# Optimization experiments

Hardware: AMD Instinct MI355X
Metric: run time of the kernel (lower is better)

Reference implementation:

```python
import jax, jax.numpy as jnp
import numpy as np

B, T, D, H = 32, 2048, 256, 256


def setup_inputs() -> dict:
    key = jax.random.key(0)
    ks = jax.random.split(key, 7)
    s = 1.0 / np.sqrt(H)  # PyTorch GRUCell default init scale
    x = jax.random.normal(ks[0], (B, T, D), jnp.float32)
    seg = jax.random.randint(ks[1], (B, T), 0, 2, jnp.int32)  # 1 = continue segment, 0 = boundary (write+reset)
    lengths = jax.random.randint(ks[2], (B,), T // 2, T, jnp.int32)
    W_ih = jax.random.uniform(ks[3], (3 * H, D), jnp.float32, -s, s)
    W_hh = jax.random.uniform(ks[4], (3 * H, H), jnp.float32, -s, s)
    b_ih = jax.random.uniform(ks[5], (3 * H,), jnp.float32, -s, s)
    b_hh = jax.random.uniform(ks[6], (3 * H,), jnp.float32, -s, s)
    return {"x": x, "seg": seg, "lengths": lengths,
            "W_ih": W_ih, "W_hh": W_hh, "b_ih": b_ih, "b_hh": b_hh}


def gru_cell(xt, h, W_ih, W_hh, b_ih, b_hh):
    # PyTorch GRUCell math
    gi = xt @ W_ih.T + b_ih          # [B, 3H]
    gh = h @ W_hh.T + b_hh           # [B, 3H]
    i_r, i_z, i_n = jnp.split(gi, 3, axis=-1)
    h_r, h_z, h_n = jnp.split(gh, 3, axis=-1)
    r = jax.nn.sigmoid(i_r + h_r)
    z = jax.nn.sigmoid(i_z + h_z)
    n = jnp.tanh(i_n + r * h_n)
    return (1.0 - z) * n + z * h


def reference(x, seg, lengths, W_ih, W_hh, b_ih, b_hh):
    Bn, Tn, _ = x.shape
    Hn = W_hh.shape[1]
    barange = jnp.arange(Bn)

    def step(carry, inp):
        h, idx, out = carry
        xt, seg_t, t = inp
        h_new = gru_cell(xt, h, W_ih, W_hh, b_ih, b_hh)
        # write h at per-example position idx where segment boundary and t < length
        write = (seg_t == 0) & (t < lengths)                     # [B] bool
        cur = out[barange, idx]                                  # [B, H]
        out = out.at[barange, idx].set(jnp.where(write[:, None], h_new, cur))
        idx = idx + write.astype(idx.dtype)
        # reset hidden to zero at segment boundaries (seg==0)
        h = seg_t.astype(h_new.dtype)[:, None] * h_new
        return (h, idx, out), None

    h0 = jnp.zeros((Bn, Hn), x.dtype)
    idx0 = jnp.zeros((Bn,), jnp.int32)
    # static max output length = Tn (original uses data-dependent max; we pad to T)
    out0 = jnp.zeros((Bn, Tn, Hn), x.dtype)
    (h, idx, out), _ = jax.lax.scan(
        step, (h0, idx0, out0),
        (jnp.transpose(x, (1, 0, 2)), seg.T, jnp.arange(Tn)))
    return out, idx
```

## Files before the change

### kernel.cpp

```cpp
#include <hip/hip_runtime.h>
#include <cstdint>
#include <cstddef>

#define TT 2048
#define BB 32
#define DD 256
#define HH 256
#define G3 768

using bf16x8 = __attribute__((ext_vector_type(8))) short;
using f32x4  = __attribute__((ext_vector_type(4))) float;

static const size_t REC_OFF = 64;
static const size_t BIH_OFF = 64 + (size_t)65536 * 16;
static const size_t BHH_OFF = BIH_OFF + (size_t)G3 * DD * 2;

__device__ __forceinline__ uint16_t f2bf(float v) {
    unsigned int u = __float_as_uint(v);
    u += 0x7FFF + ((u >> 16) & 1);
    return (uint16_t)(u >> 16);
}
__device__ __forceinline__ float bf2f(uint16_t h) {
    return __uint_as_float(((unsigned int)h) << 16);
}
__device__ __forceinline__ float sigmoidf_(float v) {
    return 1.f / (1.f + __expf(-v));
}
__device__ __forceinline__ float tanhf_(float v) {
    v = fminf(fmaxf(v, -30.f), 30.f);
    float e = __expf(-2.f * v);
    return (1.f - e) / (1.f + e);
}

__global__ void k_prep(const float* __restrict__ Wih, const float* __restrict__ Whh,
                       uint16_t* __restrict__ Bih, uint16_t* __restrict__ Bhh) {
    int i = blockIdx.x * 256 + threadIdx.x;
    if (i < G3 * DD) { Bih[i] = f2bf(Wih[i]); Bhh[i] = f2bf(Whh[i]); }
}

__global__ void k_meta(const int* __restrict__ seg, const int* __restrict__ lengths,
                       int4* __restrict__ recs, int* __restrict__ counters,
                       float* __restrict__ outIdx) {
    int b = blockIdx.x;
    int tid = threadIdx.x;
    int len = lengths[b];
    const int* s = seg + (size_t)b * TT;
    const int CH = TT / 256;
    int t0 = tid * CH;

    int cnt = 0;
    for (int t = t0; t < t0 + CH; ++t)
        cnt += (s[t] == 0 && t < len) ? 1 : 0;

    __shared__ int part[256];
    __shared__ int base;
    part[tid] = cnt;
    __syncthreads();
    if (tid == 0) {
        int run = 0;
        for (int i = 0; i < 256; ++i) { int v = part[i]; part[i] = run; run += v; }
        base = atomicAdd(&counters[0], run);
        outIdx[b] = (float)run;
    }
    __syncthreads();

    int run = part[tid];
    for (int t = t0; t < t0 + CH; ++t) {
        if (s[t] == 0 && t < len) {
            int ss = t - 1;
            while (ss >= 0 && s[ss] != 0) --ss;
            recs[base + run] = make_int4(b, ss + 1, t, run);
            ++run;
        }
    }
}

__global__ __launch_bounds__(512) void k_main(
    const float* __restrict__ x,
    const uint16_t* __restrict__ Bih, const uint16_t* __restrict__ Bhh,
    const float* __restrict__ b_ih, const float* __restrict__ b_hh,
    const int4* __restrict__ recs, int* __restrict__ counters,
    float* __restrict__ out)
{
    __shared__ __attribute__((aligned(16))) uint16_t xAhi[16 * 256];
    __shared__ __attribute__((aligned(16))) uint16_t xAlo[16 * 256];
    __shared__ __attribute__((aligned(16))) uint16_t hAhi[16 * 256];
    __shared__ __attribute__((aligned(16))) uint16_t hAlo[16 * 256];
    __shared__ int rb[16], rt[16], re[16], rp[16], alive[16];
    __shared__ int anyAliveS, nsegS;

    const int tid  = threadIdx.x;
    const int lane = tid & 63;
    const int w    = tid >> 6;
    const int lcol = lane & 15;
    const int lk8  = (lane >> 4) << 3;
    const int lrow4 = (lane >> 4) << 2;

    for (int i = tid; i < 16 * 256; i += 512) { hAhi[i] = 0; hAlo[i] = 0; }
    if (tid < 16) { alive[tid] = 0; rb[tid] = 0; rt[tid] = 0; re[tid] = -1; rp[tid] = 0; }
    if (tid == 0) nsegS = counters[0];
    __syncthreads();
    const int nseg = nsegS;

    float bR[2], bZ[2], bIN[2], bHN[2];
    #pragma unroll
    for (int ct = 0; ct < 2; ++ct) {
        int c = w * 32 + ct * 16 + lcol;
        bR[ct]  = b_ih[c]       + b_hh[c];
        bZ[ct]  = b_ih[256 + c] + b_hh[256 + c];
        bIN[ct] = b_ih[512 + c];
        bHN[ct] = b_hh[512 + c];
    }
    float hm[2][4] = {{0.f,0.f,0.f,0.f},{0.f,0.f,0.f,0.f}};

    const int srow = tid >> 5;
    const int scs  = tid & 31;

    for (;;) {
        if (tid < 16) {
            int m = tid;
            if (alive[m]) { if (rt[m] >= re[m]) alive[m] = 0; else rt[m]++; }
            if (!alive[m]) {
                int sidx = atomicAdd(&counters[1], 1);
                if (sidx < nseg) {
                    int4 r = recs[sidx];
                    rb[m] = r.x; rt[m] = r.y; re[m] = r.z; rp[m] = r.w;
                    alive[m] = 1;
                }
            }
        }
        __syncthreads();
        if (tid == 0) { int a = 0; for (int m = 0; m < 16; ++m) a |= alive[m]; anyAliveS = a; }
        if (alive[srow]) {
            const float* xp = x + ((size_t)rb[srow] * TT + rt[srow]) * DD + scs * 8;
            float4 v0 = *(const float4*)xp;
            float4 v1 = *(const float4*)(xp + 4);
            float vv[8] = {v0.x, v0.y, v0.z, v0.w, v1.x, v1.y, v1.z, v1.w};
            bf16x8 vh, vl;
            #pragma unroll
            for (int j = 0; j < 8; ++j) {
                uint16_t h = f2bf(vv[j]);
                vh[j] = (short)h;
                vl[j] = (short)f2bf(vv[j] - bf2f(h));
            }
            int base = srow * 256 + ((scs ^ (srow & 7)) << 3);
            *(bf16x8*)&xAhi[base] = vh;
            *(bf16x8*)&xAlo[base] = vl;
        }
        __syncthreads();
        if (!anyAliveS) break;

        f32x4 acc[4][2];
        #pragma unroll
        for (int g = 0; g < 4; ++g)
            #pragma unroll
            for (int ct = 0; ct < 2; ++ct)
                acc[g][ct] = (f32x4){0.f, 0.f, 0.f, 0.f};

        for (int kk = 0; kk < 8; ++kk) {
            int cs = (kk << 2) + (lane >> 4);
            int aoff = lcol * 256 + ((cs ^ (lcol & 7)) << 3);
            bf16x8 axh = *(const bf16x8*)&xAhi[aoff];
            bf16x8 axl = *(const bf16x8*)&xAlo[aoff];
            bf16x8 ahh = *(const bf16x8*)&hAhi[aoff];
            bf16x8 ahl = *(const bf16x8*)&hAlo[aoff];
            int bbase = (w * 32 + lcol) * 256 + (kk << 5) + lk8;
            #pragma unroll
            for (int g = 0; g < 3; ++g) {
                #pragma unroll
                for (int ct = 0; ct < 2; ++ct) {
                    bf16x8 bf = *(const bf16x8*)&Bih[bbase + g * 65536 + ct * 4096];
                    acc[g][ct] = __builtin_amdgcn_mfma_f32_16x16x32_bf16(axh, bf, acc[g][ct], 0, 0, 0);
                    acc[g][ct] = __builtin_amdgcn_mfma_f32_16x16x32_bf16(axl, bf, acc[g][ct], 0, 0, 0);
                }
            }
            #pragma unroll
            for (int g = 0; g < 3; ++g) {
                const int ai = (g == 2) ? 3 : g;
                #pragma unroll
                for (int ct = 0; ct < 2; ++ct) {
                    bf16x8 bf = *(const bf16x8*)&Bhh[bbase + g * 65536 + ct * 4096];
                    acc[ai][ct] = __builtin_amdgcn_mfma_f32_16x16x32_bf16(ahh, bf, acc[ai][ct], 0, 0, 0);
                    acc[ai][ct] = __builtin_amdgcn_mfma_f32_16x16x32_bf16(ahl, bf, acc[ai][ct], 0, 0, 0);
                }
            }
        }
        __syncthreads();

        #pragma unroll
        for (int ct = 0; ct < 2; ++ct) {
            int c = w * 32 + ct * 16 + lcol;
            #pragma unroll
            for (int q = 0; q < 4; ++q) {
                int row = lrow4 + q;
                float gr  = acc[0][ct][q] + bR[ct];
                float gz  = acc[1][ct][q] + bZ[ct];
                float gin = acc[2][ct][q] + bIN[ct];
                float ghn = acc[3][ct][q] + bHN[ct];
                float r = sigmoidf_(gr);
                float z = sigmoidf_(gz);
                float n = tanhf_(gin + r * ghn);
                float hnew = (1.f - z) * n + z * hm[ct][q];
                int al = alive[row];
                int em = al && (rt[row] == re[row]);
                if (em) out[((size_t)rb[row] * TT + rp[row]) * HH + c] = hnew;
                hnew = em ? 0.f : hnew;
                if (al) {
                    hm[ct][q] = hnew;
                    uint16_t hh = f2bf(hnew);
                    uint16_t hl = f2bf(hnew - bf2f(hh));
                    int idx = row * 256 + ((((c >> 3)) ^ (row & 7)) << 3) + (c & 7);
                    hAhi[idx] = hh; hAlo[idx] = hl;
                }
            }
        }
        __syncthreads();
    }
}

extern "C" void kernel_launch(void* const* d_in, const int* in_sizes, int n_in,
                              void* d_out, int out_size, void* d_ws, size_t ws_size,
                              hipStream_t stream) {
    const float* x   = (const float*)d_in[0];
    const int*   seg = (const int*)d_in[1];
    const int*   len = (const int*)d_in[2];
    const float* Wih = (const float*)d_in[3];
    const float* Whh = (const float*)d_in[4];
    const float* bih = (const float*)d_in[5];
    const float* bhh = (const float*)d_in[6];
    float* out = (float*)d_out;

    int*      counters = (int*)d_ws;
    int4*     recs     = (int4*)((char*)d_ws + REC_OFF);
    uint16_t* Bih      = (uint16_t*)((char*)d_ws + BIH_OFF);
    uint16_t* Bhh      = (uint16_t*)((char*)d_ws + BHH_OFF);

    hipMemsetAsync(d_out, 0, (size_t)out_size * sizeof(float), stream);
    hipMemsetAsync(d_ws, 0, 64, stream);

    k_prep<<<(G3 * DD + 255) / 256, 256, 0, stream>>>(Wih, Whh, Bih, Bhh);
    k_meta<<<BB, 256, 0, stream>>>(seg, len, recs, counters, out + (size_t)BB * TT * HH);
    k_main<<<512, 512, 0, stream>>>(x, Bih, Bhh, bih, bhh, recs, counters, out);
}
```

Measured before the change: 741.0 us.

## Widen GRU segment tiles to 64 rows, pre-swizzle weights, sort segments by length

Each block now processes up to 64 live segments, in four 16-row tiles, instead of 16. Every weight fragment loaded from global memory is reused across up to four MFMA row tiles, and fully dead tiles are skipped. Weights are pre-packed into a fragment-ordered layout so each lane loads contiguous data. A new single-block counting sort orders segment records longest-first to balance work across the dynamic scheduler, and slots are claimed with one atomic per wavefront. This costs 128KB of dynamic LDS, fewer blocks (256), more accumulator registers, and an extra sort kernel launch.

```diff
diff --git a/kernel.cpp b/kernel.cpp
--- a/kernel.cpp
+++ b/kernel.cpp
@@ -6,14 +6,13 @@
 #define BB 32
 #define DD 256
 #define HH 256
-#define G3 768
 
 using bf16x8 = __attribute__((ext_vector_type(8))) short;
 using f32x4  = __attribute__((ext_vector_type(4))) float;
 
-static const size_t REC_OFF = 64;
-static const size_t BIH_OFF = 64 + (size_t)65536 * 16;
-static const size_t BHH_OFF = BIH_OFF + (size_t)G3 * DD * 2;
+static const size_t REC_OFF  = 64;
+static const size_t REC2_OFF = REC_OFF  + (size_t)32768 * 16;
+static const size_t BF_OFF   = REC2_OFF + (size_t)32768 * 16;
 
 __device__ __forceinline__ uint16_t f2bf(float v) {
     unsigned int u = __float_as_uint(v);
@@ -33,9 +32,21 @@
 }
 
 __global__ void k_prep(const float* __restrict__ Wih, const float* __restrict__ Whh,
-                       uint16_t* __restrict__ Bih, uint16_t* __restrict__ Bhh) {
+                       uint16_t* __restrict__ BF) {
     int i = blockIdx.x * 256 + threadIdx.x;
-    if (i < G3 * DD) { Bih[i] = f2bf(Wih[i]); Bhh[i] = f2bf(Whh[i]); }
+    if (i >= 768 * 64) return;
+    int lane = i & 63, f = i >> 6;
+    int kk = f & 7, t = f >> 3;
+    int g = t % 6, wct = t / 6;
+    int w = wct >> 1, ct = wct & 1;
+    int col = w * 32 + ct * 16 + (lane & 15);
+    int k0 = kk * 32 + ((lane >> 4) << 3);
+    const float* W = (g < 3) ? Wih : Whh;
+    const float* src = W + (size_t)((g % 3) * 256 + col) * DD + k0;
+    bf16x8 v;
+    #pragma unroll
+    for (int e = 0; e < 8; ++e) v[e] = (short)f2bf(src[e]);
+    *(bf16x8*)&BF[(size_t)f * 512 + lane * 8] = v;
 }
 
 __global__ void k_meta(const int* __restrict__ seg, const int* __restrict__ lengths,
@@ -69,36 +80,67 @@
         if (s[t] == 0 && t < len) {
             int ss = t - 1;
             while (ss >= 0 && s[ss] != 0) --ss;
-            recs[base + run] = make_int4(b, ss + 1, t, run);
+            int slot = base + run;
+            if (slot < 32768) recs[slot] = make_int4(b, ss + 1, t, run);
             ++run;
         }
     }
 }
 
-__global__ __launch_bounds__(512) void k_main(
-    const float* __restrict__ x,
-    const uint16_t* __restrict__ Bih, const uint16_t* __restrict__ Bhh,
+__global__ void k_sort(const int4* __restrict__ recs, int4* __restrict__ recs2,
+                       const int* __restrict__ counters) {
+    __shared__ int hist[64];
+    __shared__ int off[64];
+    int n = counters[0]; if (n > 32768) n = 32768;
+    int tid = threadIdx.x;
+    if (tid < 64) hist[tid] = 0;
+    __syncthreads();
+    for (int i = tid; i < n; i += 1024) {
+        int4 r = recs[i];
+        int len = r.z - r.y + 1;
+        atomicAdd(&hist[min(len, 63)], 1);
+    }
+    __syncthreads();
+    if (tid == 0) {
+        int run = 0;
+        for (int b = 63; b >= 0; --b) { off[b] = run; run += hist[b]; }
+    }
+    __syncthreads();
+    if (tid < 64) hist[tid] = 0;
+    __syncthreads();
+    for (int i = tid; i < n; i += 1024) {
+        int4 r = recs[i];
+        int len = r.z - r.y + 1;
+        int b = min(len, 63);
+        int pos = off[b] + atomicAdd(&hist[b], 1);
+        recs2[pos] = r;
+    }
+}
+
+__global__ __launch_bounds__(512, 2) void k_main(
+    const float* __restrict__ x, const uint16_t* __restrict__ BF,
     const float* __restrict__ b_ih, const float* __restrict__ b_hh,
     const int4* __restrict__ recs, int* __restrict__ counters,
     float* __restrict__ out)
 {
-    __shared__ __attribute__((aligned(16))) uint16_t xAhi[16 * 256];
-    __shared__ __attribute__((aligned(16))) uint16_t xAlo[16 * 256];
-    __shared__ __attribute__((aligned(16))) uint16_t hAhi[16 * 256];
-    __shared__ __attribute__((aligned(16))) uint16_t hAlo[16 * 256];
-    __shared__ int rb[16], rt[16], re[16], rp[16], alive[16];
+    extern __shared__ uint16_t smem[];
+    uint16_t* xH = smem;
+    uint16_t* xL = smem + 16384;
+    uint16_t* hH = smem + 32768;
+    uint16_t* hL = smem + 49152;
+    __shared__ int rb[64], rt[64], re[64], rp[64], alive[64];
+    __shared__ int liveRTS[4];
     __shared__ int anyAliveS, nsegS;
 
     const int tid  = threadIdx.x;
     const int lane = tid & 63;
     const int w    = tid >> 6;
     const int lcol = lane & 15;
-    const int lk8  = (lane >> 4) << 3;
-    const int lrow4 = (lane >> 4) << 2;
-
-    for (int i = tid; i < 16 * 256; i += 512) { hAhi[i] = 0; hAlo[i] = 0; }
-    if (tid < 16) { alive[tid] = 0; rb[tid] = 0; rt[tid] = 0; re[tid] = -1; rp[tid] = 0; }
-    if (tid == 0) nsegS = counters[0];
+    const int lk   = lane >> 4;
+
+    for (int i = tid; i < 16384; i += 512) { hH[i] = 0; hL[i] = 0; }
+    if (tid < 64) alive[tid] = 0;
+    if (tid == 0) nsegS = min(counters[0], 32768);
     __syncthreads();
     const int nseg = nsegS;
 
@@ -111,106 +153,131 @@
         bIN[ct] = b_ih[512 + c];
         bHN[ct] = b_hh[512 + c];
     }
-    float hm[2][4] = {{0.f,0.f,0.f,0.f},{0.f,0.f,0.f,0.f}};
-
-    const int srow = tid >> 5;
-    const int scs  = tid & 31;
+    const uint16_t* BFw = BF + (size_t)w * 96 * 512;
 
     for (;;) {
-        if (tid < 16) {
+        if (tid < 64) {
             int m = tid;
-            if (alive[m]) { if (rt[m] >= re[m]) alive[m] = 0; else rt[m]++; }
-            if (!alive[m]) {
-                int sidx = atomicAdd(&counters[1], 1);
+            int al = alive[m];
+            if (al) { if (rt[m] >= re[m]) al = 0; else rt[m] = rt[m] + 1; }
+            unsigned long long deadm = __ballot(!al);
+            int base = 0;
+            if (tid == 0 && deadm) base = atomicAdd(&counters[1], __popcll(deadm));
+            base = __shfl(base, 0);
+            if (!al) {
+                int rank = __popcll(deadm & ((1ULL << tid) - 1));
+                int sidx = base + rank;
                 if (sidx < nseg) {
                     int4 r = recs[sidx];
                     rb[m] = r.x; rt[m] = r.y; re[m] = r.z; rp[m] = r.w;
-                    alive[m] = 1;
+                    al = 1;
                 }
             }
-        }
-        __syncthreads();
-        if (tid == 0) { int a = 0; for (int m = 0; m < 16; ++m) a |= alive[m]; anyAliveS = a; }
-        if (alive[srow]) {
-            const float* xp = x + ((size_t)rb[srow] * TT + rt[srow]) * DD + scs * 8;
-            float4 v0 = *(const float4*)xp;
-            float4 v1 = *(const float4*)(xp + 4);
-            float vv[8] = {v0.x, v0.y, v0.z, v0.w, v1.x, v1.y, v1.z, v1.w};
-            bf16x8 vh, vl;
-            #pragma unroll
-            for (int j = 0; j < 8; ++j) {
-                uint16_t h = f2bf(vv[j]);
-                vh[j] = (short)h;
-                vl[j] = (short)f2bf(vv[j] - bf2f(h));
-            }
-            int base = srow * 256 + ((scs ^ (srow & 7)) << 3);
-            *(bf16x8*)&xAhi[base] = vh;
-            *(bf16x8*)&xAlo[base] = vl;
+            alive[m] = al;
+            unsigned long long am = __ballot(al);
+            if (tid == 0) anyAliveS = (am != 0ULL) ? 1 : 0;
+            if (tid < 4) liveRTS[tid] = (int)((am >> (tid * 16)) & 0xFFFFULL);
         }
         __syncthreads();
         if (!anyAliveS) break;
 
-        f32x4 acc[4][2];
+        {
+            int row = tid >> 3, j = tid & 7;
+            if (alive[row]) {
+                const float* xp = x + ((size_t)rb[row] * TT + rt[row]) * DD + j * 32;
+                #pragma unroll
+                for (int u = 0; u < 4; ++u) {
+                    float4 a = *(const float4*)(xp + u * 8);
+                    float4 b = *(const float4*)(xp + u * 8 + 4);
+                    float vv[8] = {a.x, a.y, a.z, a.w, b.x, b.y, b.z, b.w};
+                    bf16x8 vh, vl;
+                    #pragma unroll
+                    for (int e = 0; e < 8; ++e) {
+                        uint16_t hi = f2bf(vv[e]);
+                        vh[e] = (short)hi;
+                        vl[e] = (short)f2bf(vv[e] - bf2f(hi));
+                    }
+                    int cs = j * 4 + u;
+                    int o = row * 256 + ((cs ^ (row & 15)) << 3);
+                    *(bf16x8*)&xH[o] = vh;
+                    *(bf16x8*)&xL[o] = vl;
+                }
+            }
+        }
+        __syncthreads();
+
+        int lv0 = liveRTS[0], lv1 = liveRTS[1], lv2 = liveRTS[2], lv3 = liveRTS[3];
+        int lv[4] = {lv0, lv1, lv2, lv3};
+
+        f32x4 acc[4][4][2];
         #pragma unroll
-        for (int g = 0; g < 4; ++g)
+        for (int rtI = 0; rtI < 4; ++rtI)
             #pragma unroll
-            for (int ct = 0; ct < 2; ++ct)
-                acc[g][ct] = (f32x4){0.f, 0.f, 0.f, 0.f};
+            for (int g = 0; g < 4; ++g)
+                #pragma unroll
+                for (int ct = 0; ct < 2; ++ct)
+                    acc[rtI][g][ct] = (f32x4){0.f, 0.f, 0.f, 0.f};
 
         for (int kk = 0; kk < 8; ++kk) {
-            int cs = (kk << 2) + (lane >> 4);
-            int aoff = lcol * 256 + ((cs ^ (lcol & 7)) << 3);
-            bf16x8 axh = *(const bf16x8*)&xAhi[aoff];
-            bf16x8 axl = *(const bf16x8*)&xAlo[aoff];
-            bf16x8 ahh = *(const bf16x8*)&hAhi[aoff];
-            bf16x8 ahl = *(const bf16x8*)&hAlo[aoff];
-            int bbase = (w * 32 + lcol) * 256 + (kk << 5) + lk8;
+            bf16x8 ax[4][2], ah[4][2];
+            int cs = kk * 4 + lk;
             #pragma unroll
-            for (int g = 0; g < 3; ++g) {
+            for (int rtI = 0; rtI < 4; ++rtI) if (lv[rtI]) {
+                int row = rtI * 16 + lcol;
+                int o = row * 256 + ((cs ^ (row & 15)) << 3);
+                ax[rtI][0] = *(const bf16x8*)&xH[o];
+                ax[rtI][1] = *(const bf16x8*)&xL[o];
+                ah[rtI][0] = *(const bf16x8*)&hH[o];
+                ah[rtI][1] = *(const bf16x8*)&hL[o];
+            }
+            #pragma unroll
+            for (int g = 0; g < 6; ++g) {
+                const int ai = (g == 0 || g == 3) ? 0 : (g == 1 || g == 4) ? 1 : (g == 2) ? 2 : 3;
                 #pragma unroll
                 for (int ct = 0; ct < 2; ++ct) {
-                    bf16x8 bf = *(const bf16x8*)&Bih[bbase + g * 65536 + ct * 4096];
-                    acc[g][ct] = __builtin_amdgcn_mfma_f32_16x16x32_bf16(axh, bf, acc[g][ct], 0, 0, 0);
-                    acc[g][ct] = __builtin_amdgcn_mfma_f32_16x16x32_bf16(axl, bf, acc[g][ct], 0, 0, 0);
+                    bf16x8 B = *(const bf16x8*)&BFw[((ct * 48 + g * 8 + kk) << 9) + (lane << 3)];
+                    #pragma unroll
+                    for (int rtI = 0; rtI < 4; ++rtI) if (lv[rtI]) {
+                        if (g < 3) {
+                            acc[rtI][ai][ct] = __builtin_amdgcn_mfma_f32_16x16x32_bf16(ax[rtI][0], B, acc[rtI][ai][ct], 0, 0, 0);
+                            acc[rtI][ai][ct] = __builtin_amdgcn_mfma_f32_16x16x32_bf16(ax[rtI][1], B, acc[rtI][ai][ct], 0, 0, 0);
+                        } else {
+                            acc[rtI][ai][ct] = __builtin_amdgcn_mfma_f32_16x16x32_bf16(ah[rtI][0], B, acc[rtI][ai][ct], 0, 0, 0);
+                            acc[rtI][ai][ct] = __builtin_amdgcn_mfma_f32_16x16x32_bf16(ah[rtI][1], B, acc[rtI][ai][ct], 0, 0, 0);
+                        }
+                    }
                 }
             }
+        }
+        __syncthreads();
+
+        #pragma unroll
+        for (int rtI = 0; rtI < 4; ++rtI) if (lv[rtI]) {
             #pragma unroll
-            for (int g = 0; g < 3; ++g) {
-                const int ai = (g == 2) ? 3 : g;
+            for (int q = 0; q < 4; ++q) {
+                int row = rtI * 16 + lk * 4 + q;
+                if (!alive[row]) continue;
+                int em = (rt[row] == re[row]);
                 #pragma unroll
                 for (int ct = 0; ct < 2; ++ct) {
-                    bf16x8 bf = *(const bf16x8*)&Bhh[bbase + g * 65536 + ct * 4096];
-                    acc[ai][ct] = __builtin_amdgcn_mfma_f32_16x16x32_bf16(ahh, bf, acc[ai][ct], 0, 0, 0);
-                    acc[ai][ct] = __builtin_amdgcn_mfma_f32_16x16x32_bf16(ahl, bf, acc[ai][ct], 0, 0, 0);
-                }
-            }
-        }
-        __syncthreads();
-
-        #pragma unroll
-        for (int ct = 0; ct < 2; ++ct) {
-            int c = w * 32 + ct * 16 + lcol;
-            #pragma unroll
-            for (int q = 0; q < 4; ++q) {
-                int row = lrow4 + q;
-                float gr  = acc[0][ct][q] + bR[ct];
-                float gz  = acc[1][ct][q] + bZ[ct];
-                float gin = acc[2][ct][q] + bIN[ct];
-                float ghn = acc[3][ct][q] + bHN[ct];
-                float r = sigmoidf_(gr);
-                float z = sigmoidf_(gz);
-                float n = tanhf_(gin + r * ghn);
-                float hnew = (1.f - z) * n + z * hm[ct][q];
-                int al = alive[row];
-                int em = al && (rt[row] == re[row]);
-                if (em) out[((size_t)rb[row] * TT + rp[row]) * HH + c] = hnew;
-                hnew = em ? 0.f : hnew;
-                if (al) {
-                    hm[ct][q] = hnew;
-                    uint16_t hh = f2bf(hnew);
-                    uint16_t hl = f2bf(hnew - bf2f(hh));
-                    int idx = row * 256 + ((((c >> 3)) ^ (row & 7)) << 3) + (c & 7);
-                    hAhi[idx] = hh; hAlo[idx] = hl;
+                    int c = w * 32 + ct * 16 + lcol;
+                    float gr  = acc[rtI][0][ct][q] + bR[ct];
+                    float gz  = acc[rtI][1][ct][q] + bZ[ct];
+                    float gin = acc[rtI][2][ct][q] + bIN[ct];
+                    float ghn = acc[rtI][3][ct][q] + bHN[ct];
+                    float rr = sigmoidf_(gr);
+                    float zz = sigmoidf_(gz);
+                    float nn = tanhf_(gin + rr * ghn);
+                    int o = row * 256 + (((c >> 3) ^ (row & 15)) << 3) + (c & 7);
+                    float hold = bf2f(hH[o]) + bf2f(hL[o]);
+                    float hnew = (1.f - zz) * nn + zz * hold;
+                    if (em) {
+                        out[((size_t)rb[row] * TT + rp[row]) * HH + c] = hnew;
+                        hnew = 0.f;
+                    }
+                    uint16_t hi = f2bf(hnew);
+                    hH[o] = hi;
+                    hL[o] = f2bf(hnew - bf2f(hi));
                 }
             }
         }
@@ -232,13 +299,21 @@
 
     int*      counters = (int*)d_ws;
     int4*     recs     = (int4*)((char*)d_ws + REC_OFF);
-    uint16_t* Bih      = (uint16_t*)((char*)d_ws + BIH_OFF);
-    uint16_t* Bhh      = (uint16_t*)((char*)d_ws + BHH_OFF);
+    int4*     recs2    = (int4*)((char*)d_ws + REC2_OFF);
+    uint16_t* BF       = (uint16_t*)((char*)d_ws + BF_OFF);
+
+    static int lds_set = 0;
+    if (!lds_set) {
+        hipFuncSetAttribute(reinterpret_cast<const void*>(&k_main),
+                            hipFuncAttributeMaxDynamicSharedMemorySize, 131072);
+        lds_set = 1;
+    }
 
     hipMemsetAsync(d_out, 0, (size_t)out_size * sizeof(float), stream);
     hipMemsetAsync(d_ws, 0, 64, stream);
 
-    k_prep<<<(G3 * DD + 255) / 256, 256, 0, stream>>>(Wih, Whh, Bih, Bhh);
+    k_prep<<<192, 256, 0, stream>>>(Wih, Whh, BF);
     k_meta<<<BB, 256, 0, stream>>>(seg, len, recs, counters, out + (size_t)BB * TT * HH);
-    k_main<<<512, 512, 0, stream>>>(x, Bih, Bhh, bih, bhh, recs, counters, out);
-}
+    k_sort<<<1, 1024, 0, stream>>>(recs, recs2, counters);
+    k_main<<<256, 512, 131072, stream>>>(x, BF, bih, bhh, recs2, counters, out);
+}
```

After: 781.6 us. 1.05x slower.
